# Kernel tuning notes

Measured on AMD Instinct MI355X. Metric: run time of the kernel, lower is better.

## Reference

```python
import jax, jax.numpy as jnp
import numpy as np
import math

D_MODEL = 2048
Q_HEAD = 32
KV_HEAD = 8
HEAD_DIM = D_MODEL // Q_HEAD  # 64
GROUP = Q_HEAD // KV_HEAD     # 4
B, T = 2, 2048


def setup_inputs() -> dict:
    key = jax.random.key(0)
    ks = jax.random.split(key, 9)
    s = 0.02
    return {
        "x": jax.random.normal(ks[0], (B, T, D_MODEL), dtype=jnp.float32),
        "Wq": jax.random.normal(ks[1], (D_MODEL, Q_HEAD * HEAD_DIM), dtype=jnp.float32) * s,
        "bq": jnp.zeros((Q_HEAD * HEAD_DIM,), dtype=jnp.float32),
        "Wk": jax.random.normal(ks[2], (D_MODEL, KV_HEAD * HEAD_DIM), dtype=jnp.float32) * s,
        "bk": jnp.zeros((KV_HEAD * HEAD_DIM,), dtype=jnp.float32),
        "Wv": jax.random.normal(ks[3], (D_MODEL, KV_HEAD * HEAD_DIM), dtype=jnp.float32) * s,
        "bv": jnp.zeros((KV_HEAD * HEAD_DIM,), dtype=jnp.float32),
        "Wo": jax.random.normal(ks[4], (D_MODEL, D_MODEL), dtype=jnp.float32) * s,
        "bo": jnp.zeros((D_MODEL,), dtype=jnp.float32),
    }


def reference(x, Wq, bq, Wk, bk, Wv, bv, Wo, bo):
    Bx, Tx, C = x.shape
    # projections -> [B, H, T, Dh]
    q = (x @ Wq + bq).reshape(Bx, Tx, Q_HEAD, HEAD_DIM).transpose(0, 2, 1, 3)
    k = (x @ Wk + bk).reshape(Bx, Tx, KV_HEAD, HEAD_DIM).transpose(0, 2, 1, 3)
    v = (x @ Wv + bv).reshape(Bx, Tx, KV_HEAD, HEAD_DIM).transpose(0, 2, 1, 3)
    # GQA: repeat each KV head `GROUP` times (repeat_interleave semantics)
    k = jnp.repeat(k, GROUP, axis=1)
    v = jnp.repeat(v, GROUP, axis=1)
    score = jnp.einsum("bhqd,bhkd->bhqk", q, k) / math.sqrt(HEAD_DIM)
    causal = jnp.tril(jnp.ones((Tx, Tx), dtype=bool))
    score = jnp.where(causal, score, -jnp.inf)
    attn = jax.nn.softmax(score, axis=-1)
    out = jnp.einsum("bhqk,bhkd->bhqd", attn, v)
    out = out.transpose(0, 2, 1, 3).reshape(Bx, Tx, C)
    return out @ Wo + bo
```

## Files before the change

kernel.cpp:

```cpp
#include <hip/hip_runtime.h>
#include <hip/hip_bf16.h>

typedef unsigned short u16;
typedef __attribute__((ext_vector_type(8)))  __bf16 bf16x8;
typedef __attribute__((ext_vector_type(8)))  unsigned short u16x8;
typedef __attribute__((ext_vector_type(4)))  unsigned short u16x4;
typedef __attribute__((ext_vector_type(4)))  float f32x4;
typedef __attribute__((ext_vector_type(16))) float f32x16;

#define MFMA(a, b, c)   __builtin_amdgcn_mfma_f32_16x16x32_bf16((a), (b), (c), 0, 0, 0)
#define MFMA32(a, b, c) __builtin_amdgcn_mfma_f32_32x32x16_bf16((a), (b), (c), 0, 0, 0)

__device__ __forceinline__ u16 f2b(float f) {
  union { float f; unsigned u; } x; x.f = f;
  unsigned r = x.u + 0x7fffu + ((x.u >> 16) & 1u);
  return (u16)(r >> 16);
}

__device__ __forceinline__ unsigned pack2(float lo, float hi) {
  const __bf16 a = (__bf16)lo, b = (__bf16)hi;
  return (unsigned)__builtin_bit_cast(u16, a) | ((unsigned)__builtin_bit_cast(u16, b) << 16);
}

__device__ __forceinline__ void gl_lds16(void* lds, const void* g) {
  __builtin_amdgcn_global_load_lds(
      (const __attribute__((address_space(1))) void*)g,
      (__attribute__((address_space(3))) void*)lds, 16, 0, 0);
}

__global__ __launch_bounds__(256) void cvt_kernel(const float* __restrict__ in,
                                                  u16* __restrict__ out, int n) {
  int i = (blockIdx.x * 256 + threadIdx.x) * 4;
  if (i >= n) return;
  f32x4 v = *(const f32x4*)(in + i);
  u16x4 o;
  o[0] = f2b(v[0]); o[1] = f2b(v[1]); o[2] = f2b(v[2]); o[3] = f2b(v[3]);
  *(u16x4*)(out + i) = o;
}

__global__ __launch_bounds__(256) void cvt_t_kernel(const float* __restrict__ W,
                                                    u16* __restrict__ Wt, int K, int N) {
  __shared__ u16 t[32][33];
  const int n0 = blockIdx.x * 32, k0 = blockIdx.y * 32;
  const int tc = threadIdx.x & 31, tr = threadIdx.x >> 5;
#pragma unroll
  for (int i = 0; i < 4; i++)
    t[tr + i * 8][tc] = f2b(W[(size_t)(k0 + tr + i * 8) * N + n0 + tc]);
  __syncthreads();
#pragma unroll
  for (int i = 0; i < 4; i++)
    Wt[(size_t)(n0 + tr + i * 8) * K + k0 + tc] = t[tc][tr + i * 8];
}

template <bool OUT_BF16>
__device__ __forceinline__ void gemm_body(const u16* __restrict__ A, const u16* __restrict__ Bt,
                                          const float* __restrict__ bias, void* __restrict__ C,
                                          const int N, const int n0, const int m0, const float scale) {
  __shared__ __align__(16) u16 As[128 * 32];
  __shared__ __align__(16) u16 Bs[128 * 32];
  const int lane = threadIdx.x & 63, wv = threadIdx.x >> 6;
  const int l15 = lane & 15, lg = lane >> 4;
  const int wm = wv >> 1, wn = wv & 1;
  const int rowQ = lane >> 2;
  const int g = lane & 3;

  f32x4 acc[4][4] = {};

  for (int k0 = 0; k0 < 2048; k0 += 32) {
#pragma unroll
    for (int c = 0; c < 2; c++) {
      const int cc = c * 4 + wv;
      const int row = cc * 16 + rowQ;
      const int gs = g ^ ((row >> 1) & 3);
      gl_lds16(&As[cc * 512], A + (((size_t)(m0 + row)) << 11) + k0 + gs * 8);
      gl_lds16(&Bs[cc * 512], Bt + (((size_t)(n0 + row)) << 11) + k0 + gs * 8);
    }
    __syncthreads();
    bf16x8 af[4], bfr[4];
#pragma unroll
    for (int t = 0; t < 4; t++) {
      const int ra = wm * 64 + t * 16 + l15;
      af[t] = *(const bf16x8*)&As[ra * 32 + ((lg ^ ((ra >> 1) & 3)) << 3)];
      const int rb = wn * 64 + t * 16 + l15;
      bfr[t] = *(const bf16x8*)&Bs[rb * 32 + ((lg ^ ((rb >> 1) & 3)) << 3)];
    }
#pragma unroll
    for (int mt = 0; mt < 4; mt++)
#pragma unroll
      for (int nt = 0; nt < 4; nt++)
        acc[mt][nt] = MFMA(af[mt], bfr[nt], acc[mt][nt]);
    __syncthreads();
  }

#pragma unroll
  for (int nt = 0; nt < 4; nt++) {
    const int col = n0 + wn * 64 + nt * 16 + l15;
    const float bc = bias[col];
#pragma unroll
    for (int mt = 0; mt < 4; mt++) {
#pragma unroll
      for (int r = 0; r < 4; r++) {
        const int row = m0 + wm * 64 + mt * 16 + lg * 4 + r;
        const float v = (acc[mt][nt][r] + bc) * scale;
        if (OUT_BF16) ((u16*)C)[(size_t)row * N + col] = f2b(v);
        else          ((float*)C)[(size_t)row * N + col] = v;
      }
    }
  }
}

__global__ __launch_bounds__(256) void qkv_gemm_kernel(
    const u16* __restrict__ xb,
    const u16* __restrict__ Wqt, const u16* __restrict__ Wkt, const u16* __restrict__ Wvt,
    const float* __restrict__ bq, const float* __restrict__ bk, const float* __restrict__ bv,
    u16* __restrict__ Qb, u16* __restrict__ Kb, u16* __restrict__ Vb) {
  const int nb = blockIdx.x;
  const u16* Bt; const float* bias; u16* out; int N, n0; float scale;
  if (nb < 16)      { Bt = Wqt; bias = bq; out = Qb; N = 2048; n0 = nb * 128;        scale = 0.125f * 1.44269504f; }
  else if (nb < 20) { Bt = Wkt; bias = bk; out = Kb; N = 512;  n0 = (nb - 16) * 128; scale = 1.0f; }
  else              { Bt = Wvt; bias = bv; out = Vb; N = 512;  n0 = (nb - 20) * 128; scale = 1.0f; }
  gemm_body<true>(xb, Bt, bias, out, N, n0, blockIdx.y * 128, scale);
}

__global__ __launch_bounds__(256) void oproj_kernel(const u16* __restrict__ Ab,
                                                    const u16* __restrict__ Wot,
                                                    const float* __restrict__ bo,
                                                    float* __restrict__ out) {
  gemm_body<false>(Ab, Wot, bo, out, 2048, blockIdx.x * 128, blockIdx.y * 128, 1.0f);
}

__global__ __launch_bounds__(512, 4) void attn_kernel(const u16* __restrict__ Qb,
                                                      const u16* __restrict__ Kb,
                                                      const u16* __restrict__ Vb,
                                                      u16* __restrict__ Ab) {
  const int i = blockIdx.x;
  const int j = i & 255;
  const int kh = j & 7, b = (j >> 3) & 1;
  const int p16 = j >> 4;
  const int qt = (i < 256) ? (31 - p16) : p16;

  const int tid = threadIdx.x;
  const int lane = tid & 63, wv = tid >> 6;
  const int hh = wv & 3, qh = wv >> 2;
  const int h = kh * 4 + hh;
  const int l31 = lane & 31, hi = lane >> 5;
  const int swz = (l31 & 7) << 3;

  __shared__ __align__(16) u16 lds[16384];
  __shared__ __align__(16) u16 Ps[8][32 * 72];

  const int skv = tid >> 3;
  const int sc8 = tid & 7;
  const int sd0 = sc8 * 8;

  const u16* Kbase = Kb + (size_t)(b * 2048) * 512 + kh * 64;
  const u16* Vbase = Vb + (size_t)(b * 2048) * 512 + kh * 64;
  u16* Pw = Ps[wv];

  const int q0 = qt * 64;

  bf16x8 qf[4];
  {
    const u16* qp = Qb + (size_t)(b * 2048 + q0 + qh * 32 + l31) * 2048 + h * 64 + hi * 8;
#pragma unroll
    for (int c = 0; c < 4; c++) qf[c] = *(const bf16x8*)(qp + c * 16);
  }
  f32x16 ot[2] = {};
  float mrow = -30000.0f, srow = 0.f;

  int cur = 0;
  {
    gl_lds16(lds + (wv << 9), Kbase + ((size_t)skv << 9) + ((sc8 ^ (skv & 7)) << 3));
    u16x8 vr = *(const u16x8*)(Vbase + ((size_t)skv << 9) + sd0);
#pragma unroll
    for (int j8 = 0; j8 < 8; j8++) {
      const int jj = (j8 + sc8) & 7;
      const int d = sd0 + jj;
      lds[8192 + d * 64 + (skv ^ ((d & 7) << 3))] = vr[jj];
    }
  }
  for (int it = 0; it <= qt; ++it) {
    __syncthreads();
    const bool pre = (it < qt);
    u16x8 vnx;
    if (pre) {
      const size_t roff = (size_t)((it + 1) * 64 + skv) << 9;
      gl_lds16(lds + ((cur ^ 1) << 12) + (wv << 9), Kbase + roff + ((sc8 ^ (skv & 7)) << 3));
      vnx = *(const u16x8*)(Vbase + roff + sd0);
    }
    const u16* Kc = lds + (cur << 12);
    const u16* Vc = lds + 8192 + (cur << 12);

    f32x16 sc2[2] = {};
#pragma unroll
    for (int c = 0; c < 4; c++) {
      const int dblk = (c * 16 + hi * 8) ^ swz;
#pragma unroll
      for (int kvh = 0; kvh < 2; kvh++) {
        bf16x8 kf = *(const bf16x8*)&Kc[(kvh * 32 + l31) * 64 + dblk];
        sc2[kvh] = MFMA32(kf, qf[c], sc2[kvh]);
      }
    }
    if (it == qt) {
      const int q = qh * 32 + l31;
#pragma unroll
      for (int kvh = 0; kvh < 2; kvh++)
#pragma unroll
        for (int r = 0; r < 16; r++) {
          const int kv = kvh * 32 + (r & 3) + 8 * (r >> 2) + 4 * hi;
          if (kv > q) sc2[kvh][r] = -30000.0f;
        }
    }
    float tm = fmaxf(sc2[0][0], sc2[0][1]);
#pragma unroll
    for (int kvh = 0; kvh < 2; kvh++)
#pragma unroll
      for (int r = (kvh ? 0 : 2); r < 16; r++) tm = fmaxf(tm, sc2[kvh][r]);
    tm = fmaxf(tm, __shfl_xor(tm, 32));
    if (__any(tm > mrow + 8.0f)) {
      const float mnew = fmaxf(mrow, tm);
      const float scl = __builtin_amdgcn_exp2f(mrow - mnew);
      mrow = mnew;
      srow *= scl;
#pragma unroll
      for (int dh = 0; dh < 2; dh++)
#pragma unroll
        for (int r = 0; r < 16; r++) ot[dh][r] *= scl;
    }
    float ps = 0.f;
#pragma unroll
    for (int kvh = 0; kvh < 2; kvh++)
#pragma unroll
      for (int j8 = 0; j8 < 8; j8++) {
        const float p0 = __builtin_amdgcn_exp2f(sc2[kvh][2 * j8] - mrow);
        const float p1 = __builtin_amdgcn_exp2f(sc2[kvh][2 * j8 + 1] - mrow);
        ps += p0 + p1;
        const int kvB = kvh * 32 + 8 * (j8 >> 1) + 2 * (j8 & 1) + 4 * hi;
        *(unsigned*)&Pw[l31 * 72 + kvB] = pack2(p0, p1);
      }
    ps += __shfl_xor(ps, 32);
    srow += ps;
#pragma unroll
    for (int t = 0; t < 4; t++) {
      const bf16x8 pf = *(const bf16x8*)&Pw[l31 * 72 + t * 16 + hi * 8];
      const int kblk = ((t * 16 + hi * 8) ^ swz);
#pragma unroll
      for (int dh = 0; dh < 2; dh++) {
        bf16x8 vf = *(const bf16x8*)&Vc[(dh * 32 + l31) * 64 + kblk];
        ot[dh] = MFMA32(vf, pf, ot[dh]);
      }
    }
    if (pre) {
#pragma unroll
      for (int j8 = 0; j8 < 8; j8++) {
        const int jj = (j8 + sc8) & 7;
        const int d = sd0 + jj;
        lds[8192 + ((cur ^ 1) << 12) + d * 64 + (skv ^ ((d & 7) << 3))] = vnx[jj];
      }
    }
    cur ^= 1;
  }
  __syncthreads();
  u16* Sx = lds + wv * 2048;
  const float inv = 1.0f / srow;
#pragma unroll
  for (int dh = 0; dh < 2; dh++)
#pragma unroll
    for (int jr = 0; jr < 8; jr++) {
      const unsigned w = pack2(ot[dh][2 * jr] * inv, ot[dh][2 * jr + 1] * inv);
      const int d = dh * 32 + 8 * (jr >> 1) + (jr & 1) * 2 + 4 * hi;
      *(unsigned*)&Sx[l31 * 64 + (d ^ swz)] = w;
    }
  __syncthreads();
#pragma unroll
  for (int rep = 0; rep < 4; rep++) {
    const int chunk = rep * 64 + lane;
    const int qr = chunk >> 3, cc = chunk & 7;
    u16x8 val = *(const u16x8*)&Sx[qr * 64 + ((cc * 8) ^ ((qr & 7) << 3))];
    *(u16x8*)&Ab[(size_t)(b * 2048 + q0 + qh * 32 + qr) * 2048 + h * 64 + cc * 8] = val;
  }
}

extern "C" void kernel_launch(void* const* d_in, const int* in_sizes, int n_in,
                              void* d_out, int out_size, void* d_ws, size_t ws_size,
                              hipStream_t stream) {
  const float* x  = (const float*)d_in[0];
  const float* Wq = (const float*)d_in[1];
  const float* bq = (const float*)d_in[2];
  const float* Wk = (const float*)d_in[3];
  const float* bk = (const float*)d_in[4];
  const float* Wv = (const float*)d_in[5];
  const float* bv = (const float*)d_in[6];
  const float* Wo = (const float*)d_in[7];
  const float* bo = (const float*)d_in[8];

  char* ws = (char*)d_ws;
  u16* xb  = (u16*)(ws + 0);
  u16* Ab  = (u16*)(ws + 0);
  u16* Qb  = (u16*)(ws + 16777216);
  u16* Kb  = (u16*)(ws + 33554432);
  u16* Vb  = (u16*)(ws + 37748736);
  u16* Wqt = (u16*)(ws + 41943040);
  u16* Wkt = (u16*)(ws + 50331648);
  u16* Wvt = (u16*)(ws + 52428800);
  u16* Wot = (u16*)(ws + 54525952);

  cvt_kernel<<<8192, 256, 0, stream>>>(x, xb, 2 * 2048 * 2048);
  cvt_t_kernel<<<dim3(64, 64), 256, 0, stream>>>(Wq, Wqt, 2048, 2048);
  cvt_t_kernel<<<dim3(16, 64), 256, 0, stream>>>(Wk, Wkt, 2048, 512);
  cvt_t_kernel<<<dim3(16, 64), 256, 0, stream>>>(Wv, Wvt, 2048, 512);
  cvt_t_kernel<<<dim3(64, 64), 256, 0, stream>>>(Wo, Wot, 2048, 2048);

  qkv_gemm_kernel<<<dim3(24, 32), 256, 0, stream>>>(xb, Wqt, Wkt, Wvt, bq, bk, bv, Qb, Kb, Vb);
  attn_kernel<<<dim3(512), 512, 0, stream>>>(Qb, Kb, Vb, Ab);
  oproj_kernel<<<dim3(16, 32), 256, 0, stream>>>(Ab, Wot, bo, (float*)d_out);
}
```

Before: 243.4 us.

## Double-buffer GEMM LDS tiles and vectorize weight transpose-convert

The GEMM main loop now uses two LDS buffers and issues the next K-tile's global-to-LDS loads before computing on the current tile. This removes one barrier per iteration and is meant to overlap load latency with MFMA work. The weight transpose kernel now uses float4 loads and u16x4 stores with a padded shared tile. The cost is twice the GEMM LDS footprint, which may lower occupancy.

```diff
diff --git a/kernel.cpp b/kernel.cpp
--- a/kernel.cpp
+++ b/kernel.cpp
@@ -40,24 +40,26 @@
 
 __global__ __launch_bounds__(256) void cvt_t_kernel(const float* __restrict__ W,
                                                     u16* __restrict__ Wt, int K, int N) {
-  __shared__ u16 t[32][33];
+  __shared__ u16 t[32][36];
   const int n0 = blockIdx.x * 32, k0 = blockIdx.y * 32;
-  const int tc = threadIdx.x & 31, tr = threadIdx.x >> 5;
-#pragma unroll
-  for (int i = 0; i < 4; i++)
-    t[tr + i * 8][tc] = f2b(W[(size_t)(k0 + tr + i * 8) * N + n0 + tc]);
+  const int r = threadIdx.x >> 3, c4 = (threadIdx.x & 7) * 4;
+  f32x4 v = *(const f32x4*)&W[(size_t)(k0 + r) * N + n0 + c4];
+  t[c4 + 0][r] = f2b(v[0]);
+  t[c4 + 1][r] = f2b(v[1]);
+  t[c4 + 2][r] = f2b(v[2]);
+  t[c4 + 3][r] = f2b(v[3]);
   __syncthreads();
-#pragma unroll
-  for (int i = 0; i < 4; i++)
-    Wt[(size_t)(n0 + tr + i * 8) * K + k0 + tc] = t[tc][tr + i * 8];
+  u16x4 o;
+  o[0] = t[r][c4]; o[1] = t[r][c4 + 1]; o[2] = t[r][c4 + 2]; o[3] = t[r][c4 + 3];
+  *(u16x4*)&Wt[(size_t)(n0 + r) * K + k0 + c4] = o;
 }
 
 template <bool OUT_BF16>
 __device__ __forceinline__ void gemm_body(const u16* __restrict__ A, const u16* __restrict__ Bt,
                                           const float* __restrict__ bias, void* __restrict__ C,
                                           const int N, const int n0, const int m0, const float scale) {
-  __shared__ __align__(16) u16 As[128 * 32];
-  __shared__ __align__(16) u16 Bs[128 * 32];
+  __shared__ __align__(16) u16 As[2][128 * 32];
+  __shared__ __align__(16) u16 Bs[2][128 * 32];
   const int lane = threadIdx.x & 63, wv = threadIdx.x >> 6;
   const int l15 = lane & 15, lg = lane >> 4;
   const int wm = wv >> 1, wn = wv & 1;
@@ -66,30 +68,36 @@
 
   f32x4 acc[4][4] = {};
 
-  for (int k0 = 0; k0 < 2048; k0 += 32) {
+  auto stage = [&](int buf, int k0) {
 #pragma unroll
     for (int c = 0; c < 2; c++) {
       const int cc = c * 4 + wv;
       const int row = cc * 16 + rowQ;
       const int gs = g ^ ((row >> 1) & 3);
-      gl_lds16(&As[cc * 512], A + (((size_t)(m0 + row)) << 11) + k0 + gs * 8);
-      gl_lds16(&Bs[cc * 512], Bt + (((size_t)(n0 + row)) << 11) + k0 + gs * 8);
-    }
+      gl_lds16(&As[buf][cc * 512], A + (((size_t)(m0 + row)) << 11) + k0 + gs * 8);
+      gl_lds16(&Bs[buf][cc * 512], Bt + (((size_t)(n0 + row)) << 11) + k0 + gs * 8);
+    }
+  };
+
+  stage(0, 0);
+  int cur = 0;
+  for (int k0 = 0; k0 < 2048; k0 += 32) {
     __syncthreads();
+    if (k0 + 32 < 2048) stage(cur ^ 1, k0 + 32);
     bf16x8 af[4], bfr[4];
 #pragma unroll
     for (int t = 0; t < 4; t++) {
       const int ra = wm * 64 + t * 16 + l15;
-      af[t] = *(const bf16x8*)&As[ra * 32 + ((lg ^ ((ra >> 1) & 3)) << 3)];
+      af[t] = *(const bf16x8*)&As[cur][ra * 32 + ((lg ^ ((ra >> 1) & 3)) << 3)];
       const int rb = wn * 64 + t * 16 + l15;
-      bfr[t] = *(const bf16x8*)&Bs[rb * 32 + ((lg ^ ((rb >> 1) & 3)) << 3)];
+      bfr[t] = *(const bf16x8*)&Bs[cur][rb * 32 + ((lg ^ ((rb >> 1) & 3)) << 3)];
     }
 #pragma unroll
     for (int mt = 0; mt < 4; mt++)
 #pragma unroll
       for (int nt = 0; nt < 4; nt++)
         acc[mt][nt] = MFMA(af[mt], bfr[nt], acc[mt][nt]);
-    __syncthreads();
+    cur ^= 1;
   }
 
 #pragma unroll
```

New measurement: 262.2 us. +7.7%, slower.
